# Performance work log

Measured on AMD Instinct MI355X. Metric: run time of the kernel, lower is better.

The kernel has to match this reference:

```python
import jax, jax.numpy as jnp
import numpy as np

NUM_EXPERTS = 64
TOP_K = 8
HIDDEN = 1024
INTER = 768
BATCH, SEQ = 1, 1024
CAPACITY = 256


def setup_inputs() -> dict:
    key = jax.random.key(0)
    k1, k2, k3, k4, k5 = jax.random.split(key, 5)
    scale = 0.02
    return {
        "hidden_states": jax.random.normal(k1, (BATCH, SEQ, HIDDEN), dtype=jnp.float32),
        "gate_w": jax.random.normal(k2, (NUM_EXPERTS, HIDDEN), dtype=jnp.float32) * scale,
        "w_gate": jax.random.normal(k3, (NUM_EXPERTS, INTER, HIDDEN), dtype=jnp.float32) * scale,
        "w_up": jax.random.normal(k4, (NUM_EXPERTS, INTER, HIDDEN), dtype=jnp.float32) * scale,
        "w_down": jax.random.normal(k5, (NUM_EXPERTS, HIDDEN, INTER), dtype=jnp.float32) * scale,
    }


def _moe_forward(hidden_states, gate_w, w_gate, w_up, w_down):
    B, S, H = hidden_states.shape
    x = hidden_states.reshape(-1, H)                      # [T, H]
    T = x.shape[0]

    # Router: linear -> float32 softmax -> top-k -> renormalize (fused in Int4MoePlugin)
    logits = (x @ gate_w.T).astype(jnp.float32)           # [T, E]
    probs = jax.nn.softmax(logits, axis=-1)
    topk_p, topk_i = jax.lax.top_k(probs, TOP_K)          # [T, K]
    topk_p = topk_p / jnp.sum(topk_p, axis=-1, keepdims=True)

    # Dispatch each (token, k) assignment into a per-expert slot (Switch-style)
    flat_e = topk_i.reshape(-1)                           # [T*K] int32
    onehot = jax.nn.one_hot(flat_e, NUM_EXPERTS, dtype=jnp.int32)
    pos_all = jnp.cumsum(onehot, axis=0) - 1              # [T*K, E]
    pos = jnp.take_along_axis(pos_all, flat_e[:, None], axis=1)[:, 0]  # [T*K]

    x_rep = jnp.repeat(x, TOP_K, axis=0)                  # [T*K, H]
    dispatch = jnp.zeros((NUM_EXPERTS, CAPACITY, H), x.dtype)
    dispatch = dispatch.at[flat_e, pos].set(x_rep, mode="drop")  # [E, C, H]

    # Grouped expert MLP: silu(x Wg^T) * (x Wu^T) then Wd^T
    g = jax.nn.silu(jnp.einsum("ech,eih->eci", dispatch, w_gate))
    u = jnp.einsum("ech,eih->eci", dispatch, w_up)
    y = jnp.einsum("eci,ehi->ech", g * u, w_down)         # [E, C, H]

    # Combine back to tokens with routing weights
    valid = (pos < CAPACITY)
    y_tok = y[flat_e, jnp.minimum(pos, CAPACITY - 1)]     # [T*K, H]
    w = (topk_p.reshape(-1) * valid.astype(topk_p.dtype)).astype(x.dtype)
    out = (y_tok * w[:, None]).reshape(T, TOP_K, H).sum(axis=1)
    return out.reshape(B, S, H)


def reference(hidden_states, gate_w, w_gate, w_up, w_down):
    return _moe_forward(hidden_states, gate_w, w_gate, w_up, w_down)
```

## Files before the change

### kernel.cpp

```cpp
#include <hip/hip_runtime.h>

#define T_TOK 1024
#define HID   1024
#define NE    64
#define TOPKK 8
#define ITR   768
#define CAP   256

typedef __attribute__((ext_vector_type(4))) float f32x4;
typedef __attribute__((ext_vector_type(8))) short s16x8;

#define OFF_COUNTS 0
#define OFF_TOPKI  1024
#define OFF_SLOT   (OFF_TOPKI + T_TOK*TOPKK*4)
#define OFF_TOPKW  (OFF_SLOT  + T_TOK*TOPKK*4)
#define OFF_ETOK   (OFF_TOPKW + T_TOK*TOPKK*4)
#define OFF_XD     (1 << 18)
#define OFF_G      (OFF_XD + (size_t)NE*CAP*HID*2)
#define OFF_Y      OFF_XD

__device__ __forceinline__ unsigned short f2bf(float f) {
  union { float f; unsigned u; } v; v.f = f;
  unsigned r = v.u + 0x7FFFu + ((v.u >> 16) & 1u);
  return (unsigned short)(r >> 16);
}
__device__ __forceinline__ float bf2f(unsigned short h) {
  union { unsigned u; float f; } v; v.u = ((unsigned)h) << 16;
  return v.f;
}
__device__ __forceinline__ unsigned pack2(float a, float b) {
  return (unsigned)f2bf(a) | ((unsigned)f2bf(b) << 16);
}

__global__ __launch_bounds__(256) void router_k(
    const float* __restrict__ x, const float* __restrict__ gw,
    int* __restrict__ topki, float* __restrict__ topkw, int* __restrict__ counts)
{
  int t = blockIdx.x, tid = threadIdx.x;
  if (t == 0 && tid < NE) counts[tid] = 0;
  __shared__ float xs[HID];
  __shared__ double parts[4 * 64];
  *(f32x4*)&xs[tid * 4] = *(const f32x4*)(x + (size_t)t * HID + tid * 4);
  __syncthreads();
  int e = tid & 63, part = tid >> 6;
  const float* g  = gw + (size_t)e * HID + part * 256;
  const float* xp = xs + part * 256;
  double acc = 0.0;
  #pragma unroll 4
  for (int h = 0; h < 256; h += 4) {
    f32x4 gv = *(const f32x4*)(g + h);
    f32x4 xv = *(const f32x4*)(xp + h);
    acc += (double)xv.x * gv.x + (double)xv.y * gv.y
         + (double)xv.z * gv.z + (double)xv.w * gv.w;
  }
  parts[part * 64 + e] = acc;
  __syncthreads();
  if (tid < 64) {
    double l = parts[tid] + parts[64 + tid] + parts[128 + tid] + parts[192 + tid];
    double m = l;
    for (int off = 32; off >= 1; off >>= 1) {
      double o = __shfl_xor(m, off, 64);
      m = o > m ? o : m;
    }
    double p  = exp(l - m);
    double pv = p;
    double wv[TOPKK]; int wi[TOPKK];
    double sum8 = 0.0;
    #pragma unroll
    for (int j = 0; j < TOPKK; ++j) {
      double bv = pv; int bi = tid;
      for (int off = 32; off >= 1; off >>= 1) {
        double ov = __shfl_xor(bv, off, 64);
        int    oi = __shfl_xor(bi, off, 64);
        if (ov > bv || (ov == bv && oi < bi)) { bv = ov; bi = oi; }
      }
      wv[j] = bv; wi[j] = bi; sum8 += bv;
      if (tid == bi) pv = -1.0;
    }
    if (tid == 0) {
      double inv = 1.0 / sum8;
      #pragma unroll
      for (int j = 0; j < TOPKK; ++j) {
        topki[t * TOPKK + j] = wi[j];
        topkw[t * TOPKK + j] = (float)(wv[j] * inv);
      }
    }
  }
}

__global__ __launch_bounds__(256) void assign_k(
    const int* __restrict__ topki, int* __restrict__ counts,
    int* __restrict__ slot_of, int* __restrict__ etok)
{
  int a = blockIdx.x * 256 + threadIdx.x;
  if (a >= T_TOK * TOPKK) return;
  int e = topki[a];
  int s = atomicAdd(counts + e, 1);
  if (s < CAP) { slot_of[a] = s; etok[e * CAP + s] = a >> 3; }
  else         { slot_of[a] = -1; }
}

__global__ __launch_bounds__(128) void dispatch_k(
    const float* __restrict__ x, const int* __restrict__ counts,
    const int* __restrict__ etok, unsigned short* __restrict__ Xd)
{
  int b = blockIdx.x;
  int e = b >> 8, s = b & 255;
  int cnt = min(counts[e], CAP);
  if (s >= cnt) return;
  int t = etok[b];
  const float* src = x + (size_t)t * HID;
  unsigned short* dst = Xd + (size_t)b * HID;
  int tid = threadIdx.x;
  #pragma unroll
  for (int i = 0; i < 2; ++i) {
    int h = (tid + i * 128) * 4;
    f32x4 v = *(const f32x4*)(src + h);
    ushort4 o;
    o.x = f2bf(v.x); o.y = f2bf(v.y); o.z = f2bf(v.z); o.w = f2bf(v.w);
    *(ushort4*)(dst + h) = o;
  }
}

__global__ __launch_bounds__(256) void gemm1_k(
    const unsigned short* __restrict__ Xd, const float* __restrict__ wg,
    const float* __restrict__ wu, const int* __restrict__ counts,
    unsigned short* __restrict__ G)
{
  int bx = blockIdx.x;
  int rt = bx & 1;
  int tmp = bx >> 1;
  int ct = tmp % 12;
  int e  = tmp / 12;
  int cnt = min(counts[e], CAP);
  if (rt * 128 >= cnt) return;

  __shared__ unsigned short As[128 * 72];
  __shared__ unsigned short Bg[64 * 72];
  __shared__ unsigned short Bu[64 * 72];

  int tid = threadIdx.x;
  int lane = tid & 63, w = tid >> 6;
  int wm = w & 1, wn = w >> 1;

  const unsigned short* Abase = Xd + ((size_t)e * CAP + rt * 128) * HID;
  const float* gbase = wg + ((size_t)e * ITR + ct * 64) * HID;
  const float* ubase = wu + ((size_t)e * ITR + ct * 64) * HID;

  f32x4 accg[4][2], accu[4][2];
  #pragma unroll
  for (int i = 0; i < 4; ++i)
    #pragma unroll
    for (int j = 0; j < 2; ++j) { accg[i][j] = (f32x4)0.0f; accu[i][j] = (f32x4)0.0f; }

  for (int kc = 0; kc < HID / 64; ++kc) {
    int k0 = kc * 64;
    __syncthreads();
    #pragma unroll
    for (int i = 0; i < 4; ++i) {
      int seg = tid + i * 256;
      int r = seg >> 3, s = seg & 7;
      uint4 v = *(const uint4*)(Abase + (size_t)r * HID + k0 + s * 8);
      *(uint4*)&As[r * 72 + s * 8] = v;
    }
    #pragma unroll
    for (int i = 0; i < 2; ++i) {
      int seg = tid + i * 256;
      int r = seg >> 3, s = seg & 7;
      const float* p = gbase + (size_t)r * HID + k0 + s * 8;
      f32x4 v0 = *(const f32x4*)p;
      f32x4 v1 = *(const f32x4*)(p + 4);
      uint4 pk;
      pk.x = pack2(v0.x, v0.y); pk.y = pack2(v0.z, v0.w);
      pk.z = pack2(v1.x, v1.y); pk.w = pack2(v1.z, v1.w);
      *(uint4*)&Bg[r * 72 + s * 8] = pk;
      p = ubase + (size_t)r * HID + k0 + s * 8;
      v0 = *(const f32x4*)p;
      v1 = *(const f32x4*)(p + 4);
      pk.x = pack2(v0.x, v0.y); pk.y = pack2(v0.z, v0.w);
      pk.z = pack2(v1.x, v1.y); pk.w = pack2(v1.z, v1.w);
      *(uint4*)&Bu[r * 72 + s * 8] = pk;
    }
    __syncthreads();
    #pragma unroll
    for (int ks = 0; ks < 2; ++ks) {
      s16x8 af[4];
      #pragma unroll
      for (int mt = 0; mt < 4; ++mt)
        af[mt] = *(const s16x8*)&As[(wm * 64 + mt * 16 + (lane & 15)) * 72 + ks * 32 + (lane >> 4) * 8];
      s16x8 bgf[2], buf_[2];
      #pragma unroll
      for (int nt = 0; nt < 2; ++nt) {
        int r = wn * 32 + nt * 16 + (lane & 15);
        bgf[nt]  = *(const s16x8*)&Bg[r * 72 + ks * 32 + (lane >> 4) * 8];
        buf_[nt] = *(const s16x8*)&Bu[r * 72 + ks * 32 + (lane >> 4) * 8];
      }
      #pragma unroll
      for (int mt = 0; mt < 4; ++mt)
        #pragma unroll
        for (int nt = 0; nt < 2; ++nt) {
          accg[mt][nt] = __builtin_amdgcn_mfma_f32_16x16x32_bf16(af[mt], bgf[nt],  accg[mt][nt], 0, 0, 0);
          accu[mt][nt] = __builtin_amdgcn_mfma_f32_16x16x32_bf16(af[mt], buf_[nt], accu[mt][nt], 0, 0, 0);
        }
    }
  }
  int rowb = rt * 128 + wm * 64;
  int colb = ct * 64 + wn * 32;
  unsigned short* Gout = G + (size_t)e * CAP * ITR;
  #pragma unroll
  for (int mt = 0; mt < 4; ++mt)
    #pragma unroll
    for (int nt = 0; nt < 2; ++nt)
      #pragma unroll
      for (int r = 0; r < 4; ++r) {
        int row = rowb + mt * 16 + (lane >> 4) * 4 + r;
        int col = colb + nt * 16 + (lane & 15);
        float gv = accg[mt][nt][r];
        float uv = accu[mt][nt][r];
        float sg = gv / (1.0f + __expf(-gv));
        Gout[(size_t)row * ITR + col] = f2bf(sg * uv);
      }
}

__global__ __launch_bounds__(256) void gemm2_k(
    const unsigned short* __restrict__ G, const float* __restrict__ wd,
    const int* __restrict__ counts, unsigned short* __restrict__ Y)
{
  int bx = blockIdx.x;
  int rt = bx & 1;
  int tmp = bx >> 1;
  int ct = tmp & 15;
  int e  = tmp >> 4;
  int cnt = min(counts[e], CAP);
  if (rt * 128 >= cnt) return;

  __shared__ unsigned short As[128 * 72];
  __shared__ unsigned short Bs[64 * 72];

  int tid = threadIdx.x;
  int lane = tid & 63, w = tid >> 6;
  int wm = w & 1, wn = w >> 1;

  const unsigned short* Abase = G + ((size_t)e * CAP + rt * 128) * ITR;
  const float* bbase = wd + ((size_t)e * HID + ct * 64) * ITR;

  f32x4 acc[4][2];
  #pragma unroll
  for (int i = 0; i < 4; ++i)
    #pragma unroll
    for (int j = 0; j < 2; ++j) acc[i][j] = (f32x4)0.0f;

  for (int kc = 0; kc < ITR / 64; ++kc) {
    int k0 = kc * 64;
    __syncthreads();
    #pragma unroll
    for (int i = 0; i < 4; ++i) {
      int seg = tid + i * 256;
      int r = seg >> 3, s = seg & 7;
      uint4 v = *(const uint4*)(Abase + (size_t)r * ITR + k0 + s * 8);
      *(uint4*)&As[r * 72 + s * 8] = v;
    }
    #pragma unroll
    for (int i = 0; i < 2; ++i) {
      int seg = tid + i * 256;
      int r = seg >> 3, s = seg & 7;
      const float* p = bbase + (size_t)r * ITR + k0 + s * 8;
      f32x4 v0 = *(const f32x4*)p;
      f32x4 v1 = *(const f32x4*)(p + 4);
      uint4 pk;
      pk.x = pack2(v0.x, v0.y); pk.y = pack2(v0.z, v0.w);
      pk.z = pack2(v1.x, v1.y); pk.w = pack2(v1.z, v1.w);
      *(uint4*)&Bs[r * 72 + s * 8] = pk;
    }
    __syncthreads();
    #pragma unroll
    for (int ks = 0; ks < 2; ++ks) {
      s16x8 af[4];
      #pragma unroll
      for (int mt = 0; mt < 4; ++mt)
        af[mt] = *(const s16x8*)&As[(wm * 64 + mt * 16 + (lane & 15)) * 72 + ks * 32 + (lane >> 4) * 8];
      s16x8 bf[2];
      #pragma unroll
      for (int nt = 0; nt < 2; ++nt) {
        int r = wn * 32 + nt * 16 + (lane & 15);
        bf[nt] = *(const s16x8*)&Bs[r * 72 + ks * 32 + (lane >> 4) * 8];
      }
      #pragma unroll
      for (int mt = 0; mt < 4; ++mt)
        #pragma unroll
        for (int nt = 0; nt < 2; ++nt)
          acc[mt][nt] = __builtin_amdgcn_mfma_f32_16x16x32_bf16(af[mt], bf[nt], acc[mt][nt], 0, 0, 0);
    }
  }
  int rowb = rt * 128 + wm * 64;
  int colb = ct * 64 + wn * 32;
  unsigned short* Yout = Y + (size_t)e * CAP * HID;
  #pragma unroll
  for (int mt = 0; mt < 4; ++mt)
    #pragma unroll
    for (int nt = 0; nt < 2; ++nt)
      #pragma unroll
      for (int r = 0; r < 4; ++r) {
        int row = rowb + mt * 16 + (lane >> 4) * 4 + r;
        int col = colb + nt * 16 + (lane & 15);
        Yout[(size_t)row * HID + col] = f2bf(acc[mt][nt][r]);
      }
}

__global__ __launch_bounds__(256) void combine_k(
    const unsigned short* __restrict__ Y, const int* __restrict__ topki,
    const int* __restrict__ slot_of, const float* __restrict__ topkw,
    float* __restrict__ out)
{
  int t = blockIdx.x, tid = threadIdx.x;
  int h = tid * 4;
  float a0 = 0.f, a1 = 0.f, a2 = 0.f, a3 = 0.f;
  #pragma unroll
  for (int k = 0; k < TOPKK; ++k) {
    int a = t * TOPKK + k;
    int s = slot_of[a];
    if (s < 0) continue;
    int e = topki[a];
    float wt = topkw[a];
    const unsigned short* yp = Y + ((size_t)(e * CAP + s)) * HID + h;
    ushort4 yv = *(const ushort4*)yp;
    a0 += wt * bf2f(yv.x);
    a1 += wt * bf2f(yv.y);
    a2 += wt * bf2f(yv.z);
    a3 += wt * bf2f(yv.w);
  }
  f32x4 o = { a0, a1, a2, a3 };
  *(f32x4*)(out + (size_t)t * HID + h) = o;
}

extern "C" void kernel_launch(void* const* d_in, const int* in_sizes, int n_in,
                              void* d_out, int out_size, void* d_ws, size_t ws_size,
                              hipStream_t stream)
{
  const float* x     = (const float*)d_in[0];
  const float* gw    = (const float*)d_in[1];
  const float* wgate = (const float*)d_in[2];
  const float* wup   = (const float*)d_in[3];
  const float* wdown = (const float*)d_in[4];
  float* out = (float*)d_out;

  char* ws = (char*)d_ws;
  int*   counts  = (int*)  (ws + OFF_COUNTS);
  int*   topki   = (int*)  (ws + OFF_TOPKI);
  int*   slot_of = (int*)  (ws + OFF_SLOT);
  float* topkw   = (float*)(ws + OFF_TOPKW);
  int*   etok    = (int*)  (ws + OFF_ETOK);
  unsigned short* Xd = (unsigned short*)(ws + OFF_XD);
  unsigned short* G  = (unsigned short*)(ws + OFF_G);
  unsigned short* Y  = (unsigned short*)(ws + OFF_Y);

  router_k  <<<T_TOK, 256, 0, stream>>>(x, gw, topki, topkw, counts);
  assign_k  <<<(T_TOK * TOPKK) / 256, 256, 0, stream>>>(topki, counts, slot_of, etok);
  dispatch_k<<<NE * CAP, 128, 0, stream>>>(x, counts, etok, Xd);
  gemm1_k   <<<NE * 12 * 2, 256, 0, stream>>>(Xd, wgate, wup, counts, G);
  gemm2_k   <<<NE * 16 * 2, 256, 0, stream>>>(G, wdown, counts, Y);
  combine_k <<<T_TOK, 256, 0, stream>>>(Y, topki, slot_of, topkw, out);
}
```

Measured before the change: 676.1 us.

## Retile expert GEMMs to full-capacity row tiles with direct-to-LDS loads and prefetch

Each expert GEMM block now covers the whole capacity (up to 256 rows) for a 64-column slice, so each fp32 weight tile is read and converted to bf16 once per expert instead of once per 128-row tile. The activation tile is loaded straight into LDS with global_load_lds and an XOR swizzle replaces the padded layout. The next weight tile is prefetched into registers while MFMAs run, and warps whose row range is beyond the expert's count skip compute. In exchange the grid is half as large, each block uses more LDS and more accumulator registers, and occupancy hints are added via launch bounds.

New measurement: 612.6 us. 9.4% less time.

```diff
diff --git a/kernel.cpp b/kernel.cpp
--- a/kernel.cpp
+++ b/kernel.cpp
@@ -30,6 +30,12 @@
 }
 __device__ __forceinline__ unsigned pack2(float a, float b) {
   return (unsigned)f2bf(a) | ((unsigned)f2bf(b) << 16);
+}
+
+__device__ __forceinline__ void gld_lds16(const unsigned short* g, unsigned short* l) {
+  __builtin_amdgcn_global_load_lds(
+      (const __attribute__((address_space(1))) unsigned int*)g,
+      (__attribute__((address_space(3))) unsigned int*)l, 16, 0, 0);
 }
 
 __global__ __launch_bounds__(256) void router_k(
@@ -122,189 +128,226 @@
   }
 }
 
-__global__ __launch_bounds__(256) void gemm1_k(
+__global__ __launch_bounds__(256, 2) void gemm1_k(
     const unsigned short* __restrict__ Xd, const float* __restrict__ wg,
     const float* __restrict__ wu, const int* __restrict__ counts,
     unsigned short* __restrict__ G)
 {
   int bx = blockIdx.x;
-  int rt = bx & 1;
-  int tmp = bx >> 1;
-  int ct = tmp % 12;
-  int e  = tmp / 12;
+  int ct = bx % 12;
+  int e  = bx / 12;
   int cnt = min(counts[e], CAP);
-  if (rt * 128 >= cnt) return;
-
-  __shared__ unsigned short As[128 * 72];
-  __shared__ unsigned short Bg[64 * 72];
-  __shared__ unsigned short Bu[64 * 72];
+  if (cnt <= 0) return;
+  int ru = (cnt + 63) & ~63;
+
+  __shared__ unsigned short As[CAP * 64];
+  __shared__ unsigned short Bg[64 * 64];
+  __shared__ unsigned short Bu[64 * 64];
 
   int tid = threadIdx.x;
   int lane = tid & 63, w = tid >> 6;
-  int wm = w & 1, wn = w >> 1;
-
-  const unsigned short* Abase = Xd + ((size_t)e * CAP + rt * 128) * HID;
+  bool wactive = (w * 64) < ru;
+
+  const unsigned short* Abase = Xd + (size_t)e * CAP * HID;
   const float* gbase = wg + ((size_t)e * ITR + ct * 64) * HID;
   const float* ubase = wu + ((size_t)e * ITR + ct * 64) * HID;
 
-  f32x4 accg[4][2], accu[4][2];
+  int br = tid >> 3;
+  int bs = tid & 7;
+
+  f32x4 pg[2][2], pu[2][2];
+  #pragma unroll
+  for (int j = 0; j < 2; ++j) {
+    const float* p0 = gbase + (size_t)(br + j * 32) * HID + bs * 8;
+    pg[j][0] = *(const f32x4*)p0;  pg[j][1] = *(const f32x4*)(p0 + 4);
+    const float* p1 = ubase + (size_t)(br + j * 32) * HID + bs * 8;
+    pu[j][0] = *(const f32x4*)p1;  pu[j][1] = *(const f32x4*)(p1 + 4);
+  }
+
+  f32x4 accg[4][4], accu[4][4];
   #pragma unroll
   for (int i = 0; i < 4; ++i)
     #pragma unroll
-    for (int j = 0; j < 2; ++j) { accg[i][j] = (f32x4)0.0f; accu[i][j] = (f32x4)0.0f; }
+    for (int j = 0; j < 4; ++j) { accg[i][j] = (f32x4)0.0f; accu[i][j] = (f32x4)0.0f; }
 
   for (int kc = 0; kc < HID / 64; ++kc) {
     int k0 = kc * 64;
     __syncthreads();
     #pragma unroll
-    for (int i = 0; i < 4; ++i) {
-      int seg = tid + i * 256;
-      int r = seg >> 3, s = seg & 7;
-      uint4 v = *(const uint4*)(Abase + (size_t)r * HID + k0 + s * 8);
-      *(uint4*)&As[r * 72 + s * 8] = v;
-    }
-    #pragma unroll
-    for (int i = 0; i < 2; ++i) {
-      int seg = tid + i * 256;
-      int r = seg >> 3, s = seg & 7;
-      const float* p = gbase + (size_t)r * HID + k0 + s * 8;
-      f32x4 v0 = *(const f32x4*)p;
-      f32x4 v1 = *(const f32x4*)(p + 4);
+    for (int i = 0; i < 8; ++i) {
+      if (i * 32 < ru) {
+        int q = tid + i * 256;
+        int r = q >> 3, s = q & 7;
+        int ss = s ^ (r & 7);
+        gld_lds16(Abase + (size_t)r * HID + k0 + ss * 8, &As[q * 8]);
+      }
+    }
+    #pragma unroll
+    for (int j = 0; j < 2; ++j) {
+      int r = br + j * 32;
+      int sw = bs ^ (r & 7);
       uint4 pk;
-      pk.x = pack2(v0.x, v0.y); pk.y = pack2(v0.z, v0.w);
-      pk.z = pack2(v1.x, v1.y); pk.w = pack2(v1.z, v1.w);
-      *(uint4*)&Bg[r * 72 + s * 8] = pk;
-      p = ubase + (size_t)r * HID + k0 + s * 8;
-      v0 = *(const f32x4*)p;
-      v1 = *(const f32x4*)(p + 4);
-      pk.x = pack2(v0.x, v0.y); pk.y = pack2(v0.z, v0.w);
-      pk.z = pack2(v1.x, v1.y); pk.w = pack2(v1.z, v1.w);
-      *(uint4*)&Bu[r * 72 + s * 8] = pk;
+      pk.x = pack2(pg[j][0].x, pg[j][0].y); pk.y = pack2(pg[j][0].z, pg[j][0].w);
+      pk.z = pack2(pg[j][1].x, pg[j][1].y); pk.w = pack2(pg[j][1].z, pg[j][1].w);
+      *(uint4*)&Bg[r * 64 + sw * 8] = pk;
+      pk.x = pack2(pu[j][0].x, pu[j][0].y); pk.y = pack2(pu[j][0].z, pu[j][0].w);
+      pk.z = pack2(pu[j][1].x, pu[j][1].y); pk.w = pack2(pu[j][1].z, pu[j][1].w);
+      *(uint4*)&Bu[r * 64 + sw * 8] = pk;
     }
     __syncthreads();
-    #pragma unroll
-    for (int ks = 0; ks < 2; ++ks) {
-      s16x8 af[4];
-      #pragma unroll
-      for (int mt = 0; mt < 4; ++mt)
-        af[mt] = *(const s16x8*)&As[(wm * 64 + mt * 16 + (lane & 15)) * 72 + ks * 32 + (lane >> 4) * 8];
-      s16x8 bgf[2], buf_[2];
-      #pragma unroll
-      for (int nt = 0; nt < 2; ++nt) {
-        int r = wn * 32 + nt * 16 + (lane & 15);
-        bgf[nt]  = *(const s16x8*)&Bg[r * 72 + ks * 32 + (lane >> 4) * 8];
-        buf_[nt] = *(const s16x8*)&Bu[r * 72 + ks * 32 + (lane >> 4) * 8];
-      }
-      #pragma unroll
-      for (int mt = 0; mt < 4; ++mt)
-        #pragma unroll
-        for (int nt = 0; nt < 2; ++nt) {
-          accg[mt][nt] = __builtin_amdgcn_mfma_f32_16x16x32_bf16(af[mt], bgf[nt],  accg[mt][nt], 0, 0, 0);
-          accu[mt][nt] = __builtin_amdgcn_mfma_f32_16x16x32_bf16(af[mt], buf_[nt], accu[mt][nt], 0, 0, 0);
-        }
-    }
-  }
-  int rowb = rt * 128 + wm * 64;
-  int colb = ct * 64 + wn * 32;
-  unsigned short* Gout = G + (size_t)e * CAP * ITR;
-  #pragma unroll
-  for (int mt = 0; mt < 4; ++mt)
-    #pragma unroll
-    for (int nt = 0; nt < 2; ++nt)
-      #pragma unroll
-      for (int r = 0; r < 4; ++r) {
-        int row = rowb + mt * 16 + (lane >> 4) * 4 + r;
-        int col = colb + nt * 16 + (lane & 15);
-        float gv = accg[mt][nt][r];
-        float uv = accu[mt][nt][r];
-        float sg = gv / (1.0f + __expf(-gv));
-        Gout[(size_t)row * ITR + col] = f2bf(sg * uv);
-      }
-}
-
-__global__ __launch_bounds__(256) void gemm2_k(
+    if (kc + 1 < HID / 64) {
+      int k1 = k0 + 64;
+      #pragma unroll
+      for (int j = 0; j < 2; ++j) {
+        const float* p0 = gbase + (size_t)(br + j * 32) * HID + k1 + bs * 8;
+        pg[j][0] = *(const f32x4*)p0;  pg[j][1] = *(const f32x4*)(p0 + 4);
+        const float* p1 = ubase + (size_t)(br + j * 32) * HID + k1 + bs * 8;
+        pu[j][0] = *(const f32x4*)p1;  pu[j][1] = *(const f32x4*)(p1 + 4);
+      }
+    }
+    if (wactive) {
+      #pragma unroll
+      for (int ks = 0; ks < 2; ++ks) {
+        int t = ks * 4 + (lane >> 4);
+        s16x8 af[4];
+        #pragma unroll
+        for (int mt = 0; mt < 4; ++mt) {
+          int R = w * 64 + mt * 16 + (lane & 15);
+          af[mt] = *(const s16x8*)&As[R * 64 + (t ^ (R & 7)) * 8];
+        }
+        #pragma unroll
+        for (int nt = 0; nt < 4; ++nt) {
+          int rB = nt * 16 + (lane & 15);
+          int sB = (t ^ (rB & 7)) * 8;
+          s16x8 bg = *(const s16x8*)&Bg[rB * 64 + sB];
+          s16x8 bu = *(const s16x8*)&Bu[rB * 64 + sB];
+          #pragma unroll
+          for (int mt = 0; mt < 4; ++mt) {
+            accg[mt][nt] = __builtin_amdgcn_mfma_f32_16x16x32_bf16(af[mt], bg, accg[mt][nt], 0, 0, 0);
+            accu[mt][nt] = __builtin_amdgcn_mfma_f32_16x16x32_bf16(af[mt], bu, accu[mt][nt], 0, 0, 0);
+          }
+        }
+      }
+    }
+  }
+  if (wactive) {
+    unsigned short* Gout = G + (size_t)e * CAP * ITR;
+    #pragma unroll
+    for (int mt = 0; mt < 4; ++mt)
+      #pragma unroll
+      for (int nt = 0; nt < 4; ++nt)
+        #pragma unroll
+        for (int r = 0; r < 4; ++r) {
+          int row = w * 64 + mt * 16 + (lane >> 4) * 4 + r;
+          int col = ct * 64 + nt * 16 + (lane & 15);
+          float gv = accg[mt][nt][r];
+          float uv = accu[mt][nt][r];
+          float sg = gv / (1.0f + __expf(-gv));
+          Gout[(size_t)row * ITR + col] = f2bf(sg * uv);
+        }
+  }
+}
+
+__global__ __launch_bounds__(256, 3) void gemm2_k(
     const unsigned short* __restrict__ G, const float* __restrict__ wd,
     const int* __restrict__ counts, unsigned short* __restrict__ Y)
 {
   int bx = blockIdx.x;
-  int rt = bx & 1;
-  int tmp = bx >> 1;
-  int ct = tmp & 15;
-  int e  = tmp >> 4;
+  int ct = bx & 15;
+  int e  = bx >> 4;
   int cnt = min(counts[e], CAP);
-  if (rt * 128 >= cnt) return;
-
-  __shared__ unsigned short As[128 * 72];
-  __shared__ unsigned short Bs[64 * 72];
+  if (cnt <= 0) return;
+  int ru = (cnt + 63) & ~63;
+
+  __shared__ unsigned short As[CAP * 64];
+  __shared__ unsigned short Bs[64 * 64];
 
   int tid = threadIdx.x;
   int lane = tid & 63, w = tid >> 6;
-  int wm = w & 1, wn = w >> 1;
-
-  const unsigned short* Abase = G + ((size_t)e * CAP + rt * 128) * ITR;
+  bool wactive = (w * 64) < ru;
+
+  const unsigned short* Abase = G + (size_t)e * CAP * ITR;
   const float* bbase = wd + ((size_t)e * HID + ct * 64) * ITR;
 
-  f32x4 acc[4][2];
+  int br = tid >> 3, bs = tid & 7;
+
+  f32x4 pb[2][2];
+  #pragma unroll
+  for (int j = 0; j < 2; ++j) {
+    const float* p0 = bbase + (size_t)(br + j * 32) * ITR + bs * 8;
+    pb[j][0] = *(const f32x4*)p0;  pb[j][1] = *(const f32x4*)(p0 + 4);
+  }
+
+  f32x4 acc[4][4];
   #pragma unroll
   for (int i = 0; i < 4; ++i)
     #pragma unroll
-    for (int j = 0; j < 2; ++j) acc[i][j] = (f32x4)0.0f;
+    for (int j = 0; j < 4; ++j) acc[i][j] = (f32x4)0.0f;
 
   for (int kc = 0; kc < ITR / 64; ++kc) {
     int k0 = kc * 64;
     __syncthreads();
     #pragma unroll
-    for (int i = 0; i < 4; ++i) {
-      int seg = tid + i * 256;
-      int r = seg >> 3, s = seg & 7;
-      uint4 v = *(const uint4*)(Abase + (size_t)r * ITR + k0 + s * 8);
-      *(uint4*)&As[r * 72 + s * 8] = v;
-    }
-    #pragma unroll
-    for (int i = 0; i < 2; ++i) {
-      int seg = tid + i * 256;
-      int r = seg >> 3, s = seg & 7;
-      const float* p = bbase + (size_t)r * ITR + k0 + s * 8;
-      f32x4 v0 = *(const f32x4*)p;
-      f32x4 v1 = *(const f32x4*)(p + 4);
+    for (int i = 0; i < 8; ++i) {
+      if (i * 32 < ru) {
+        int q = tid + i * 256;
+        int r = q >> 3, s = q & 7;
+        int ss = s ^ (r & 7);
+        gld_lds16(Abase + (size_t)r * ITR + k0 + ss * 8, &As[q * 8]);
+      }
+    }
+    #pragma unroll
+    for (int j = 0; j < 2; ++j) {
+      int r = br + j * 32;
+      int sw = bs ^ (r & 7);
       uint4 pk;
-      pk.x = pack2(v0.x, v0.y); pk.y = pack2(v0.z, v0.w);
-      pk.z = pack2(v1.x, v1.y); pk.w = pack2(v1.z, v1.w);
-      *(uint4*)&Bs[r * 72 + s * 8] = pk;
+      pk.x = pack2(pb[j][0].x, pb[j][0].y); pk.y = pack2(pb[j][0].z, pb[j][0].w);
+      pk.z = pack2(pb[j][1].x, pb[j][1].y); pk.w = pack2(pb[j][1].z, pb[j][1].w);
+      *(uint4*)&Bs[r * 64 + sw * 8] = pk;
     }
     __syncthreads();
-    #pragma unroll
-    for (int ks = 0; ks < 2; ++ks) {
-      s16x8 af[4];
-      #pragma unroll
-      for (int mt = 0; mt < 4; ++mt)
-        af[mt] = *(const s16x8*)&As[(wm * 64 + mt * 16 + (lane & 15)) * 72 + ks * 32 + (lane >> 4) * 8];
-      s16x8 bf[2];
-      #pragma unroll
-      for (int nt = 0; nt < 2; ++nt) {
-        int r = wn * 32 + nt * 16 + (lane & 15);
-        bf[nt] = *(const s16x8*)&Bs[r * 72 + ks * 32 + (lane >> 4) * 8];
-      }
-      #pragma unroll
-      for (int mt = 0; mt < 4; ++mt)
-        #pragma unroll
-        for (int nt = 0; nt < 2; ++nt)
-          acc[mt][nt] = __builtin_amdgcn_mfma_f32_16x16x32_bf16(af[mt], bf[nt], acc[mt][nt], 0, 0, 0);
-    }
-  }
-  int rowb = rt * 128 + wm * 64;
-  int colb = ct * 64 + wn * 32;
-  unsigned short* Yout = Y + (size_t)e * CAP * HID;
-  #pragma unroll
-  for (int mt = 0; mt < 4; ++mt)
-    #pragma unroll
-    for (int nt = 0; nt < 2; ++nt)
-      #pragma unroll
-      for (int r = 0; r < 4; ++r) {
-        int row = rowb + mt * 16 + (lane >> 4) * 4 + r;
-        int col = colb + nt * 16 + (lane & 15);
-        Yout[(size_t)row * HID + col] = f2bf(acc[mt][nt][r]);
-      }
+    if (kc + 1 < ITR / 64) {
+      int k1 = k0 + 64;
+      #pragma unroll
+      for (int j = 0; j < 2; ++j) {
+        const float* p0 = bbase + (size_t)(br + j * 32) * ITR + k1 + bs * 8;
+        pb[j][0] = *(const f32x4*)p0;  pb[j][1] = *(const f32x4*)(p0 + 4);
+      }
+    }
+    if (wactive) {
+      #pragma unroll
+      for (int ks = 0; ks < 2; ++ks) {
+        int t = ks * 4 + (lane >> 4);
+        s16x8 af[4];
+        #pragma unroll
+        for (int mt = 0; mt < 4; ++mt) {
+          int R = w * 64 + mt * 16 + (lane & 15);
+          af[mt] = *(const s16x8*)&As[R * 64 + (t ^ (R & 7)) * 8];
+        }
+        #pragma unroll
+        for (int nt = 0; nt < 4; ++nt) {
+          int rB = nt * 16 + (lane & 15);
+          s16x8 bf = *(const s16x8*)&Bs[rB * 64 + (t ^ (rB & 7)) * 8];
+          #pragma unroll
+          for (int mt = 0; mt < 4; ++mt)
+            acc[mt][nt] = __builtin_amdgcn_mfma_f32_16x16x32_bf16(af[mt], bf, acc[mt][nt], 0, 0, 0);
+        }
+      }
+    }
+  }
+  if (wactive) {
+    unsigned short* Yout = Y + (size_t)e * CAP * HID;
+    #pragma unroll
+    for (int mt = 0; mt < 4; ++mt)
+      #pragma unroll
+      for (int nt = 0; nt < 4; ++nt)
+        #pragma unroll
+        for (int r = 0; r < 4; ++r) {
+          int row = w * 64 + mt * 16 + (lane >> 4) * 4 + r;
+          int col = ct * 64 + nt * 16 + (lane & 15);
+          Yout[(size_t)row * HID + col] = f2bf(acc[mt][nt][r]);
+        }
+  }
 }
 
 __global__ __launch_bounds__(256) void combine_k(
@@ -357,7 +400,7 @@
   router_k  <<<T_TOK, 256, 0, stream>>>(x, gw, topki, topkw, counts);
   assign_k  <<<(T_TOK * TOPKK) / 256, 256, 0, stream>>>(topki, counts, slot_of, etok);
   dispatch_k<<<NE * CAP, 128, 0, stream>>>(x, counts, etok, Xd);
-  gemm1_k   <<<NE * 12 * 2, 256, 0, stream>>>(Xd, wgate, wup, counts, G);
-  gemm2_k   <<<NE * 16 * 2, 256, 0, stream>>>(G, wdown, counts, Y);
+  gemm1_k   <<<NE * 12, 256, 0, stream>>>(Xd, wgate, wup, counts, G);
+  gemm2_k   <<<NE * 16, 256, 0, stream>>>(G, wdown, counts, Y);
   combine_k <<<T_TOK, 256, 0, stream>>>(Y, topki, slot_of, topkw, out);
 }
```
